# Kernel tuning notes

Hardware: AMD Instinct MI355X
Metric: run time of the kernel (lower is better)

## Reference

```python
import jax, jax.numpy as jnp
import numpy as np

# Key observation: the TF module groups ROIs per image (boolean_mask), runs the
# same MLP on each group, concatenates the ragged results, then argsort-gathers
# to restore the ORIGINAL row order. Since the Dense/ReLU MLP acts row-wise and
# identically for every image, the group -> MLP -> regroup pipeline is exactly
# equivalent to applying the MLP to all rows in their original order. The clean
# JAX reference therefore computes the same math with a single fused GEMM chain.

NUM_CLASSES = 81
HIDDEN_DIM = 1024
N = 2048          # total ROIs
SS = 7            # sample_size
FS = 256          # feature_size
FEAT_DIM = SS * SS * FS  # 12544
NUM_IMAGES = 8


def setup_inputs() -> dict:
    key = jax.random.key(0)
    ks = jax.random.split(key, 8)
    features = jax.random.normal(ks[0], (N, SS, SS, FS), dtype=jnp.float32)
    batch_indices = jnp.sort(jax.random.randint(ks[1], (N,), 0, NUM_IMAGES, dtype=jnp.int32))
    s1 = 1.0 / np.sqrt(FEAT_DIM)
    s2 = 1.0 / np.sqrt(HIDDEN_DIM)
    W1 = jax.random.uniform(ks[2], (FEAT_DIM, HIDDEN_DIM), jnp.float32, -s1, s1)
    b1 = jnp.zeros((HIDDEN_DIM,), jnp.float32)
    W2 = jax.random.uniform(ks[3], (HIDDEN_DIM, HIDDEN_DIM), jnp.float32, -s2, s2)
    b2 = jnp.zeros((HIDDEN_DIM,), jnp.float32)
    Wc = jax.random.uniform(ks[4], (HIDDEN_DIM, NUM_CLASSES), jnp.float32, -s2, s2)
    bc = jnp.zeros((NUM_CLASSES,), jnp.float32)
    return {"features": features, "batch_indices": batch_indices,
            "W1": W1, "b1": b1, "W2": W2, "b2": b2, "Wc": Wc, "bc": bc}


def reference(features, batch_indices, W1, b1, W2, b2, Wc, bc):
    # Group/ungroup in the original is an identity permutation on rows, but we
    # reproduce it explicitly and cheaply: stable-sort rows by image id, run the
    # MLP, then invert the permutation via argsort (same as TF argsort-gather).
    order = jnp.argsort(batch_indices, stable=True)          # group rows per image
    x = features[order].reshape(features.shape[0], -1)       # [N, feat_dim]
    x = jax.nn.relu(x @ W1 + b1)
    x = jax.nn.relu(x @ W2 + b2)
    logits = x @ Wc + bc                                     # [N, num_classes]
    inv = jnp.argsort(order)                                 # restore original order
    return logits[inv]
```

## Files before the change

### kernel.cpp

```cpp
#include <hip/hip_runtime.h>
#include <hip/hip_bf16.h>
#include <stdint.h>

typedef __bf16 bf16_t;
typedef __bf16 bf16x4 __attribute__((ext_vector_type(4)));
typedef __bf16 bf16x8 __attribute__((ext_vector_type(8)));
typedef float f32x4 __attribute__((ext_vector_type(4)));

#define BM 128
#define BN 128
#define BK 32

__device__ __forceinline__ void async_ld16(const bf16_t* g, bf16_t* lds) {
    __builtin_amdgcn_global_load_lds(
        (__attribute__((address_space(1))) void*)g,
        (__attribute__((address_space(3))) void*)lds,
        16, 0, 0);
}


__global__ void cvt4_f32_bf16(const float* __restrict__ in, bf16_t* __restrict__ out, int n4) {
    int i = blockIdx.x * 256 + threadIdx.x;
    if (i >= n4) return;
    float4 v = ((const float4*)in)[i];
    bf16x4 o = { (bf16_t)v.x, (bf16_t)v.y, (bf16_t)v.z, (bf16_t)v.w };
    ((bf16x4*)out)[i] = o;
}

__global__ void transpose_cvt(const float* __restrict__ in, bf16_t* __restrict__ out,
                              int R, int C, int Cp) {
    __shared__ float tile[32][33];
    const int c0 = blockIdx.x * 32;
    const int r0 = blockIdx.y * 32;
    const int tx = threadIdx.x;
    const int ty = threadIdx.y;
#pragma unroll
    for (int i = 0; i < 32; i += 8) {
        int rr = r0 + ty + i, cc = c0 + tx;
        float v = 0.f;
        if (rr < R && cc < C) v = in[(size_t)rr * C + cc];
        tile[ty + i][tx] = v;
    }
    __syncthreads();
#pragma unroll
    for (int i = 0; i < 32; i += 8) {
        int oc = c0 + ty + i;
        int orr = r0 + tx;
        if (oc < Cp && orr < R)
            out[(size_t)oc * R + orr] = (bf16_t)tile[tx][ty + i];
    }
}

__global__ __launch_bounds__(256) void gemm_bf16(
    const bf16_t* __restrict__ A, const bf16_t* __restrict__ B,
    float* __restrict__ P, int M, int N, int K, int Kchunk)
{
    __shared__ __align__(16) bf16_t Asm[BM * BK];
    __shared__ __align__(16) bf16_t Bsm[BN * BK];

    const int tid  = threadIdx.x;
    const int wave = tid >> 6;
    const int lane = tid & 63;
    const int bm = blockIdx.x, bn = blockIdx.y, s = blockIdx.z;

    const bf16_t* Ab = A + (size_t)bm * BM * K + (size_t)s * Kchunk;
    const bf16_t* Bb = B + (size_t)bn * BN * K + (size_t)s * Kchunk;

    const int ar = lane >> 2;
    const int ak = (lane & 3) * 8;

    const int wm = (wave >> 1) * 64;
    const int wn = (wave & 1) * 64;
    const int kq = (lane >> 4) * 8;
    const int r  = lane & 15;

    f32x4 acc[4][4];
#pragma unroll
    for (int i = 0; i < 4; ++i)
#pragma unroll
        for (int j = 0; j < 4; ++j)
            acc[i][j] = f32x4{0.f, 0.f, 0.f, 0.f};

    for (int k0 = 0; k0 < Kchunk; k0 += BK) {
        __syncthreads();
#pragma unroll
        for (int i = 0; i < 2; ++i) {
            const int rb = (wave * 2 + i) * 16;
            async_ld16(Ab + (size_t)(rb + ar) * K + (k0 + ak), &Asm[rb * BK]);
            async_ld16(Bb + (size_t)(rb + ar) * K + (k0 + ak), &Bsm[rb * BK]);
        }
        __syncthreads();

        bf16x8 af[4], bfr[4];
#pragma unroll
        for (int i = 0; i < 4; ++i)
            af[i] = *(const bf16x8*)&Asm[(wm + i * 16 + r) * BK + kq];
#pragma unroll
        for (int j = 0; j < 4; ++j)
            bfr[j] = *(const bf16x8*)&Bsm[(wn + j * 16 + r) * BK + kq];
#pragma unroll
        for (int i = 0; i < 4; ++i)
#pragma unroll
            for (int j = 0; j < 4; ++j)
                acc[i][j] = __builtin_amdgcn_mfma_f32_16x16x32_bf16(af[i], bfr[j], acc[i][j], 0, 0, 0);
    }

    float* Pb = P + ((size_t)s * M + (size_t)bm * BM) * N + (size_t)bn * BN;
    const int r4 = (lane >> 4) * 4;
    const int c  = lane & 15;
#pragma unroll
    for (int i = 0; i < 4; ++i)
#pragma unroll
        for (int j = 0; j < 4; ++j)
#pragma unroll
            for (int rg = 0; rg < 4; ++rg)
                Pb[(size_t)(wm + i * 16 + r4 + rg) * N + (wn + j * 16 + c)] = acc[i][j][rg];
}


__global__ void reduce_relu_bf16_k(const float* __restrict__ P, const float* __restrict__ bias,
                                   bf16_t* __restrict__ h, int S, int MN, int Nm1) {
    int i4 = (blockIdx.x * 256 + threadIdx.x) * 4;
    if (i4 >= MN) return;
    int n = i4 & Nm1;
    float4 a = *(const float4*)(bias + n);
    for (int s = 0; s < S; ++s) {
        float4 p = *(const float4*)(P + (size_t)s * MN + i4);
        a.x += p.x; a.y += p.y; a.z += p.z; a.w += p.w;
    }
    a.x = fmaxf(a.x, 0.f); a.y = fmaxf(a.y, 0.f);
    a.z = fmaxf(a.z, 0.f); a.w = fmaxf(a.w, 0.f);
    bf16x4 o = { (bf16_t)a.x, (bf16_t)a.y, (bf16_t)a.z, (bf16_t)a.w };
    *(bf16x4*)(h + i4) = o;
}

__global__ void reduce_out_k(const float* __restrict__ P, const float* __restrict__ bc,
                             float* __restrict__ out, int M, int NC, int NCP) {
    int idx = blockIdx.x * 256 + threadIdx.x;
    if (idx >= M * NC) return;
    int m = idx / NC;
    int n = idx - m * NC;
    out[idx] = P[(size_t)m * NCP + n] + bc[n];
}


extern "C" void kernel_launch(void* const* d_in, const int* in_sizes, int n_in,
                              void* d_out, int out_size, void* d_ws, size_t ws_size,
                              hipStream_t stream) {
    const float* X  = (const float*)d_in[0];
    const float* W1 = (const float*)d_in[2];
    const float* b1 = (const float*)d_in[3];
    const float* W2 = (const float*)d_in[4];
    const float* b2 = (const float*)d_in[5];
    const float* Wc = (const float*)d_in[6];
    const float* bc = (const float*)d_in[7];
    float* out = (float*)d_out;

    const int M    = in_sizes[1];
    const int FEAT = in_sizes[0] / M;
    const int HID  = in_sizes[3];
    const int NC   = in_sizes[7];
    const int NCP  = 128;

    char* ws = (char*)d_ws;
    size_t off = 0;
    auto alloc = [&](size_t bytes) {
        char* p = ws + off;
        off += (bytes + 255) & ~(size_t)255;
        return p;
    };
    bf16_t* Xb  = (bf16_t*)alloc((size_t)M * FEAT * 2);
    bf16_t* W1T = (bf16_t*)alloc((size_t)FEAT * HID * 2);
    bf16_t* W2T = (bf16_t*)alloc((size_t)HID * HID * 2);
    bf16_t* WcT = (bf16_t*)alloc((size_t)NCP * HID * 2);
    bf16_t* h1  = (bf16_t*)alloc((size_t)M * HID * 2);
    bf16_t* h2  = (bf16_t*)alloc((size_t)M * HID * 2);
    float*  P   = (float*)(ws + off);

    size_t rem  = ws_size > off ? ws_size - off : 0;
    size_t perS = (size_t)M * HID * 4;
    int S1 = (rem >= 4 * perS) ? 4 : (rem >= 2 * perS ? 2 : 1);
    int S2 = (S1 >= 2) ? 2 : 1;

    int n4 = (M * FEAT) / 4;
    cvt4_f32_bf16<<<(n4 + 255) / 256, 256, 0, stream>>>(X, Xb, n4);
    dim3 tt(32, 8);
    transpose_cvt<<<dim3(HID / 32, FEAT / 32), tt, 0, stream>>>(W1, W1T, FEAT, HID, HID);
    transpose_cvt<<<dim3(HID / 32, HID / 32), tt, 0, stream>>>(W2, W2T, HID, HID, HID);
    transpose_cvt<<<dim3(NCP / 32, HID / 32), tt, 0, stream>>>(Wc, WcT, HID, NC, NCP);

    gemm_bf16<<<dim3(M / BM, HID / BN, S1), 256, 0, stream>>>(Xb, W1T, P, M, HID, FEAT, FEAT / S1);
    reduce_relu_bf16_k<<<(M * HID / 4 + 255) / 256, 256, 0, stream>>>(P, b1, h1, S1, M * HID, HID - 1);

    gemm_bf16<<<dim3(M / BM, HID / BN, S2), 256, 0, stream>>>(h1, W2T, P, M, HID, HID, HID / S2);
    reduce_relu_bf16_k<<<(M * HID / 4 + 255) / 256, 256, 0, stream>>>(P, b2, h2, S2, M * HID, HID - 1);

    gemm_bf16<<<dim3(M / BM, NCP / BN, 1), 256, 0, stream>>>(h2, WcT, P, M, NCP, HID, HID);
    reduce_out_k<<<(M * NC + 255) / 256, 256, 0, stream>>>(P, bc, out, M, NC, NCP);
}
```

Measured before the change: 353.1 us.

## Fuse prep kernels, raise split-K factors, and split-K the classifier GEMM

Merges the input conversion and three weight transposes into a single launch to cut launch overhead. Raises the split-K depth for the first two GEMMs (up to 8 and 4) and adds split-K of 8 to the classifier GEMM, which previously launched only 16 blocks. The reduce kernels are templated on the split count so their loops unroll. More split-K partials mean more fp32 partial-sum traffic in the reductions. The transpose bounds checks were partly dropped, which assumes dimensions divisible by 32.

```diff
diff --git a/kernel.cpp b/kernel.cpp
--- a/kernel.cpp
+++ b/kernel.cpp
@@ -19,26 +19,20 @@
 }
 
 
-__global__ void cvt4_f32_bf16(const float* __restrict__ in, bf16_t* __restrict__ out, int n4) {
-    int i = blockIdx.x * 256 + threadIdx.x;
-    if (i >= n4) return;
-    float4 v = ((const float4*)in)[i];
-    bf16x4 o = { (bf16_t)v.x, (bf16_t)v.y, (bf16_t)v.z, (bf16_t)v.w };
-    ((bf16x4*)out)[i] = o;
-}
-
-__global__ void transpose_cvt(const float* __restrict__ in, bf16_t* __restrict__ out,
-                              int R, int C, int Cp) {
-    __shared__ float tile[32][33];
-    const int c0 = blockIdx.x * 32;
-    const int r0 = blockIdx.y * 32;
-    const int tx = threadIdx.x;
-    const int ty = threadIdx.y;
+__device__ __forceinline__ void transpose_tile(
+    const float* __restrict__ in, bf16_t* __restrict__ out,
+    int R, int C, int Cp, int tileIdx, int tid, float (*tile)[33])
+{
+    const int tilesX = Cp / 32;
+    const int c0 = (tileIdx % tilesX) * 32;
+    const int r0 = (tileIdx / tilesX) * 32;
+    const int tx = tid & 31;
+    const int ty = tid >> 5;
 #pragma unroll
     for (int i = 0; i < 32; i += 8) {
         int rr = r0 + ty + i, cc = c0 + tx;
         float v = 0.f;
-        if (rr < R && cc < C) v = in[(size_t)rr * C + cc];
+        if (cc < C) v = in[(size_t)rr * C + cc];
         tile[ty + i][tx] = v;
     }
     __syncthreads();
@@ -46,9 +40,35 @@
     for (int i = 0; i < 32; i += 8) {
         int oc = c0 + ty + i;
         int orr = r0 + tx;
-        if (oc < Cp && orr < R)
-            out[(size_t)oc * R + orr] = (bf16_t)tile[tx][ty + i];
-    }
+        out[(size_t)oc * R + orr] = (bf16_t)tile[tx][ty + i];
+    }
+}
+
+__global__ void prep_all(const float* __restrict__ X, bf16_t* __restrict__ Xb, int n4,
+                         const float* __restrict__ W1, bf16_t* __restrict__ W1T,
+                         const float* __restrict__ W2, bf16_t* __restrict__ W2T,
+                         const float* __restrict__ Wc, bf16_t* __restrict__ WcT,
+                         int FEAT, int HID, int NC, int NCP,
+                         int nCvt, int t1, int t2)
+{
+    __shared__ float tile[32][33];
+    int bid = blockIdx.x;
+    int tid = threadIdx.x;
+    if (bid < nCvt) {
+        int i = bid * 256 + tid;
+        if (i < n4) {
+            float4 v = ((const float4*)X)[i];
+            bf16x4 o = { (bf16_t)v.x, (bf16_t)v.y, (bf16_t)v.z, (bf16_t)v.w };
+            ((bf16x4*)Xb)[i] = o;
+        }
+        return;
+    }
+    bid -= nCvt;
+    if (bid < t1) { transpose_tile(W1, W1T, FEAT, HID, HID, bid, tid, tile); return; }
+    bid -= t1;
+    if (bid < t2) { transpose_tile(W2, W2T, HID, HID, HID, bid, tid, tile); return; }
+    bid -= t2;
+    transpose_tile(Wc, WcT, HID, NC, NCP, bid, tid, tile);
 }
 
 __global__ __launch_bounds__(256) void gemm_bf16(
@@ -118,12 +138,14 @@
 }
 
 
+template <int S>
 __global__ void reduce_relu_bf16_k(const float* __restrict__ P, const float* __restrict__ bias,
-                                   bf16_t* __restrict__ h, int S, int MN, int Nm1) {
+                                   bf16_t* __restrict__ h, int MN, int Nm1) {
     int i4 = (blockIdx.x * 256 + threadIdx.x) * 4;
     if (i4 >= MN) return;
     int n = i4 & Nm1;
     float4 a = *(const float4*)(bias + n);
+#pragma unroll
     for (int s = 0; s < S; ++s) {
         float4 p = *(const float4*)(P + (size_t)s * MN + i4);
         a.x += p.x; a.y += p.y; a.z += p.z; a.w += p.w;
@@ -134,13 +156,19 @@
     *(bf16x4*)(h + i4) = o;
 }
 
+template <int S>
 __global__ void reduce_out_k(const float* __restrict__ P, const float* __restrict__ bc,
                              float* __restrict__ out, int M, int NC, int NCP) {
     int idx = blockIdx.x * 256 + threadIdx.x;
     if (idx >= M * NC) return;
     int m = idx / NC;
     int n = idx - m * NC;
-    out[idx] = P[(size_t)m * NCP + n] + bc[n];
+    float a = bc[n];
+    size_t MN = (size_t)M * NCP;
+#pragma unroll
+    for (int s = 0; s < S; ++s)
+        a += P[s * MN + (size_t)m * NCP + n];
+    out[idx] = a;
 }
 
 
@@ -179,22 +207,33 @@
 
     size_t rem  = ws_size > off ? ws_size - off : 0;
     size_t perS = (size_t)M * HID * 4;
-    int S1 = (rem >= 4 * perS) ? 4 : (rem >= 2 * perS ? 2 : 1);
-    int S2 = (S1 >= 2) ? 2 : 1;
-
-    int n4 = (M * FEAT) / 4;
-    cvt4_f32_bf16<<<(n4 + 255) / 256, 256, 0, stream>>>(X, Xb, n4);
-    dim3 tt(32, 8);
-    transpose_cvt<<<dim3(HID / 32, FEAT / 32), tt, 0, stream>>>(W1, W1T, FEAT, HID, HID);
-    transpose_cvt<<<dim3(HID / 32, HID / 32), tt, 0, stream>>>(W2, W2T, HID, HID, HID);
-    transpose_cvt<<<dim3(NCP / 32, HID / 32), tt, 0, stream>>>(Wc, WcT, HID, NC, NCP);
+    int S1 = (rem >= 8 * perS) ? 8 : (rem >= 4 * perS) ? 4 : (rem >= 2 * perS) ? 2 : 1;
+    int S2 = (S1 >= 4) ? 4 : S1;
+    const int S3 = 8;
+
+    int n4   = (M * FEAT) / 4;
+    int nCvt = (n4 + 255) / 256;
+    int t1 = (HID / 32) * (FEAT / 32);
+    int t2 = (HID / 32) * (HID / 32);
+    int t3 = (NCP / 32) * (HID / 32);
+    prep_all<<<nCvt + t1 + t2 + t3, 256, 0, stream>>>(
+        X, Xb, n4, W1, W1T, W2, W2T, Wc, WcT, FEAT, HID, NC, NCP, nCvt, t1, t2);
 
     gemm_bf16<<<dim3(M / BM, HID / BN, S1), 256, 0, stream>>>(Xb, W1T, P, M, HID, FEAT, FEAT / S1);
-    reduce_relu_bf16_k<<<(M * HID / 4 + 255) / 256, 256, 0, stream>>>(P, b1, h1, S1, M * HID, HID - 1);
+    switch (S1) {
+        case 8: reduce_relu_bf16_k<8><<<(M * HID / 4 + 255) / 256, 256, 0, stream>>>(P, b1, h1, M * HID, HID - 1); break;
+        case 4: reduce_relu_bf16_k<4><<<(M * HID / 4 + 255) / 256, 256, 0, stream>>>(P, b1, h1, M * HID, HID - 1); break;
+        case 2: reduce_relu_bf16_k<2><<<(M * HID / 4 + 255) / 256, 256, 0, stream>>>(P, b1, h1, M * HID, HID - 1); break;
+        default: reduce_relu_bf16_k<1><<<(M * HID / 4 + 255) / 256, 256, 0, stream>>>(P, b1, h1, M * HID, HID - 1); break;
+    }
 
     gemm_bf16<<<dim3(M / BM, HID / BN, S2), 256, 0, stream>>>(h1, W2T, P, M, HID, HID, HID / S2);
-    reduce_relu_bf16_k<<<(M * HID / 4 + 255) / 256, 256, 0, stream>>>(P, b2, h2, S2, M * HID, HID - 1);
-
-    gemm_bf16<<<dim3(M / BM, NCP / BN, 1), 256, 0, stream>>>(h2, WcT, P, M, NCP, HID, HID);
-    reduce_out_k<<<(M * NC + 255) / 256, 256, 0, stream>>>(P, bc, out, M, NC, NCP);
-}
+    switch (S2) {
+        case 4: reduce_relu_bf16_k<4><<<(M * HID / 4 + 255) / 256, 256, 0, stream>>>(P, b2, h2, M * HID, HID - 1); break;
+        case 2: reduce_relu_bf16_k<2><<<(M * HID / 4 + 255) / 256, 256, 0, stream>>>(P, b2, h2, M * HID, HID - 1); break;
+        default: reduce_relu_bf16_k<1><<<(M * HID / 4 + 255) / 256, 256, 0, stream>>>(P, b2, h2, M * HID, HID - 1); break;
+    }
+
+    gemm_bf16<<<dim3(M / BM, NCP / BN, S3), 256, 0, stream>>>(h2, WcT, P, M, NCP, HID, HID / S3);
+    reduce_out_k<S3><<<(M * NC + 255) / 256, 256, 0, stream>>>(P, bc, out, M, NC, NCP);
+}
```

Result: faster. 323.8 us (-8.3%).
